# Kernel optimization log

Hardware: AMD Instinct MI355X
Metric: run time of the kernel (lower is better)

The kernel has to match this reference:

```python
import jax, jax.numpy as jnp
import numpy as np


def setup_inputs() -> dict:
    key = jax.random.key(0)
    k1, k2 = jax.random.split(key)
    mat_1 = jax.random.normal(k1, (8192, 128), dtype=jnp.float32)
    mat_2 = jax.random.normal(k2, (8192, 128), dtype=jnp.float32)
    return {"mat_1": mat_1, "mat_2": mat_2}


def reference(mat_1, mat_2):
    # Squared Euclidean distance between every row of mat_1 and every row of mat_2.
    # Same math as sum((mat_1[i] - mat_2[j])**2) but expressed via the
    # ||a||^2 + ||b||^2 - 2 a.b identity so the [n1, n2, d] intermediate is
    # never materialized (single GEMM + rank-1 broadcasts).
    sq1 = jnp.sum(mat_1 * mat_1, axis=1, keepdims=True)        # [n1, 1]
    sq2 = jnp.sum(mat_2 * mat_2, axis=1)                        # [n2]
    cross = jnp.einsum('id,jd->ij', mat_1, mat_2)               # [n1, n2]
    return sq1 + sq2[None, :] - 2.0 * cross
```

## Files before the change

### kernel.cpp

```cpp
#include <hip/hip_runtime.h>


typedef __attribute__((ext_vector_type(8))) short bf16x8;
typedef __attribute__((ext_vector_type(4))) float f32x4;

__device__ __forceinline__ short f2bf(float f) {
    union { float f; unsigned u; } x; x.f = f;
    unsigned r = x.u + 0x7FFFu + ((x.u >> 16) & 1u);
    return (short)(r >> 16);
}

__global__ void norms_kernel(const float* __restrict__ m1,
                             const float* __restrict__ m2,
                             float* __restrict__ n1,
                             float* __restrict__ n2,
                             int rows1, int rows2) {
    int gwave = (int)((blockIdx.x * blockDim.x + threadIdx.x) >> 6);
    int lane  = threadIdx.x & 63;
    const float* src;
    float* dst;
    int row;
    if (gwave < rows1) { src = m1; dst = n1; row = gwave; }
    else {
        row = gwave - rows1;
        if (row >= rows2) return;
        src = m2; dst = n2;
    }
    const float2* p = (const float2*)(src + (size_t)row * 128);
    float2 v = p[lane];
    float s = v.x * v.x + v.y * v.y;
#pragma unroll
    for (int off = 32; off; off >>= 1) s += __shfl_xor(s, off, 64);
    if (lane == 0) dst[row] = s;
}

#define BM 128
#define BN 128
#define BK 64

__global__ __launch_bounds__(256, 3)
void dist_kernel(const float* __restrict__ A, const float* __restrict__ B,
                 const float* __restrict__ n1, const float* __restrict__ n2,
                 float* __restrict__ out, int N2) {
    __shared__ short As[BM][BK];
    __shared__ short Bs[BN][BK];

    const int tid  = threadIdx.x;
    const int wave = tid >> 6;
    const int lane = tid & 63;
    const int q    = lane >> 4;
    const int l15  = lane & 15;

    const int ti = blockIdx.y * BM;
    const int tj = blockIdx.x * BN;

    const int wm = (wave >> 1) * 64;
    const int wn = (wave & 1) * 64;

    f32x4 acc[4][4] = {};

    for (int kc = 0; kc < 128; kc += BK) {
#pragma unroll
        for (int g = 0; g < 4; ++g) {
            int idx = tid + g * 256;
            int row = idx >> 3;
            int kg  = (idx & 7) * 8;
            const float4* pa = (const float4*)(A + (size_t)(ti + row) * 128 + kc + kg);
            float4 v0 = pa[0], v1 = pa[1];
            bf16x8 w;
            w[0] = f2bf(v0.x); w[1] = f2bf(v0.y); w[2] = f2bf(v0.z); w[3] = f2bf(v0.w);
            w[4] = f2bf(v1.x); w[5] = f2bf(v1.y); w[6] = f2bf(v1.z); w[7] = f2bf(v1.w);
            *(bf16x8*)&As[row][kg] = w;
        }
#pragma unroll
        for (int g = 0; g < 4; ++g) {
            int idx = tid + g * 256;
            int row = idx >> 3;
            int kg  = (idx & 7) * 8;
            const float4* pb = (const float4*)(B + (size_t)(tj + row) * 128 + kc + kg);
            float4 v0 = pb[0], v1 = pb[1];
            bf16x8 w;
            w[0] = f2bf(v0.x); w[1] = f2bf(v0.y); w[2] = f2bf(v0.z); w[3] = f2bf(v0.w);
            w[4] = f2bf(v1.x); w[5] = f2bf(v1.y); w[6] = f2bf(v1.z); w[7] = f2bf(v1.w);
            *(bf16x8*)&Bs[row][kg] = w;
        }
        __syncthreads();

#pragma unroll
        for (int kk = 0; kk < BK; kk += 32) {
            bf16x8 af[4], bfr[4];
#pragma unroll
            for (int mi = 0; mi < 4; ++mi)
                af[mi] = *(const bf16x8*)&As[wm + mi * 16 + l15][kk + q * 8];
#pragma unroll
            for (int ni = 0; ni < 4; ++ni)
                bfr[ni] = *(const bf16x8*)&Bs[wn + ni * 16 + l15][kk + q * 8];
#pragma unroll
            for (int mi = 0; mi < 4; ++mi)
#pragma unroll
                for (int ni = 0; ni < 4; ++ni)
                    acc[mi][ni] = __builtin_amdgcn_mfma_f32_16x16x32_bf16(
                        af[mi], bfr[ni], acc[mi][ni], 0, 0, 0);
        }
        __syncthreads();
    }

#pragma unroll
    for (int mi = 0; mi < 4; ++mi) {
        int r0 = ti + wm + mi * 16 + q * 4;
        float a0 = n1[r0 + 0], a1 = n1[r0 + 1], a2 = n1[r0 + 2], a3 = n1[r0 + 3];
#pragma unroll
        for (int ni = 0; ni < 4; ++ni) {
            int c = tj + wn + ni * 16 + l15;
            float nb = n2[c];
            f32x4 v = acc[mi][ni];
            out[(size_t)(r0 + 0) * N2 + c] = a0 + nb - 2.0f * v[0];
            out[(size_t)(r0 + 1) * N2 + c] = a1 + nb - 2.0f * v[1];
            out[(size_t)(r0 + 2) * N2 + c] = a2 + nb - 2.0f * v[2];
            out[(size_t)(r0 + 3) * N2 + c] = a3 + nb - 2.0f * v[3];
        }
    }
}

extern "C" void kernel_launch(void* const* d_in, const int* in_sizes, int n_in,
                              void* d_out, int out_size, void* d_ws, size_t ws_size,
                              hipStream_t stream) {
    const float* m1 = (const float*)d_in[0];
    const float* m2 = (const float*)d_in[1];
    float* out = (float*)d_out;
    const int rows1 = in_sizes[0] / 128;
    const int rows2 = in_sizes[1] / 128;

    float* n1 = (float*)d_ws;
    float* n2 = n1 + rows1;

    int total_waves = rows1 + rows2;
    int nb = (total_waves * 64 + 255) / 256;
    norms_kernel<<<nb, 256, 0, stream>>>(m1, m2, n1, n2, rows1, rows2);

    dim3 grid(rows2 / BN, rows1 / BM);
    dist_kernel<<<grid, 256, 0, stream>>>(m1, m2, n1, n2, out, rows2);
}
```

Baseline: 272.6 us.

## Pre-convert inputs to bf16 in prep kernel and stage tiles via direct global-to-LDS loads

The norms kernel now also writes bf16 copies of both input matrices into the workspace. The distance kernel then loads those copies straight into shared memory with global_load_lds, which drops the per-tile fp32 loads, the conversion arithmetic and the register round trip. Because each input row is re-read by 64 tiles, this halves the bytes fetched per tile and frees VGPRs. In exchange it costs an extra 4MB of bf16 writes in the prep pass and hardcodes the output row stride at 8192.

New measurement: 285.9 us. +4.9%, slower.

```diff
diff --git a/kernel.cpp b/kernel.cpp
--- a/kernel.cpp
+++ b/kernel.cpp
@@ -4,34 +4,38 @@
 typedef __attribute__((ext_vector_type(8))) short bf16x8;
 typedef __attribute__((ext_vector_type(4))) float f32x4;
 
-__device__ __forceinline__ short f2bf(float f) {
+typedef __attribute__((address_space(1))) const void gvoid_t;
+typedef __attribute__((address_space(3))) void lvoid_t;
+
+__device__ __forceinline__ unsigned short f2bf(float f) {
     union { float f; unsigned u; } x; x.f = f;
     unsigned r = x.u + 0x7FFFu + ((x.u >> 16) & 1u);
-    return (short)(r >> 16);
+    return (unsigned short)(r >> 16);
 }
 
-__global__ void norms_kernel(const float* __restrict__ m1,
-                             const float* __restrict__ m2,
-                             float* __restrict__ n1,
-                             float* __restrict__ n2,
-                             int rows1, int rows2) {
+__global__ void prep_kernel(const float* __restrict__ m1,
+                            const float* __restrict__ m2,
+                            unsigned short* __restrict__ A2,
+                            unsigned short* __restrict__ B2,
+                            float* __restrict__ n1,
+                            float* __restrict__ n2,
+                            int rows1, int rows2) {
     int gwave = (int)((blockIdx.x * blockDim.x + threadIdx.x) >> 6);
     int lane  = threadIdx.x & 63;
-    const float* src;
-    float* dst;
-    int row;
-    if (gwave < rows1) { src = m1; dst = n1; row = gwave; }
+    const float* src; unsigned short* dst; float* nd; int row;
+    if (gwave < rows1) { src = m1; dst = A2; nd = n1; row = gwave; }
     else {
         row = gwave - rows1;
         if (row >= rows2) return;
-        src = m2; dst = n2;
+        src = m2; dst = B2; nd = n2;
     }
-    const float2* p = (const float2*)(src + (size_t)row * 128);
-    float2 v = p[lane];
+    float2 v = ((const float2*)(src + (size_t)row * 128))[lane];
     float s = v.x * v.x + v.y * v.y;
+    ushort2 w; w.x = f2bf(v.x); w.y = f2bf(v.y);
+    ((ushort2*)(dst + (size_t)row * 128))[lane] = w;
 #pragma unroll
     for (int off = 32; off; off >>= 1) s += __shfl_xor(s, off, 64);
-    if (lane == 0) dst[row] = s;
+    if (lane == 0) nd[row] = s;
 }
 
 #define BM 128
@@ -39,11 +43,12 @@
 #define BK 64
 
 __global__ __launch_bounds__(256, 3)
-void dist_kernel(const float* __restrict__ A, const float* __restrict__ B,
+void dist_kernel(const unsigned short* __restrict__ A2,
+                 const unsigned short* __restrict__ B2,
                  const float* __restrict__ n1, const float* __restrict__ n2,
-                 float* __restrict__ out, int N2) {
-    __shared__ short As[BM][BK];
-    __shared__ short Bs[BN][BK];
+                 float* __restrict__ out) {
+    __shared__ __align__(16) unsigned short As[BM * BK];
+    __shared__ __align__(16) unsigned short Bs[BN * BK];
 
     const int tid  = threadIdx.x;
     const int wave = tid >> 6;
@@ -57,32 +62,27 @@
     const int wm = (wave >> 1) * 64;
     const int wn = (wave & 1) * 64;
 
+    const int srow   = lane >> 3;
+    const int schunk = lane & 7;
+
     f32x4 acc[4][4] = {};
 
     for (int kc = 0; kc < 128; kc += BK) {
 #pragma unroll
-        for (int g = 0; g < 4; ++g) {
-            int idx = tid + g * 256;
-            int row = idx >> 3;
-            int kg  = (idx & 7) * 8;
-            const float4* pa = (const float4*)(A + (size_t)(ti + row) * 128 + kc + kg);
-            float4 v0 = pa[0], v1 = pa[1];
-            bf16x8 w;
-            w[0] = f2bf(v0.x); w[1] = f2bf(v0.y); w[2] = f2bf(v0.z); w[3] = f2bf(v0.w);
-            w[4] = f2bf(v1.x); w[5] = f2bf(v1.y); w[6] = f2bf(v1.z); w[7] = f2bf(v1.w);
-            *(bf16x8*)&As[row][kg] = w;
+        for (int t = 0; t < 4; ++t) {
+            int i = wave * 4 + t;
+            int row = i * 8 + srow;
+            const unsigned short* g = A2 + (size_t)(ti + row) * 128 + kc + schunk * 8;
+            unsigned short* l = As + i * 512;
+            __builtin_amdgcn_global_load_lds((gvoid_t*)g, (lvoid_t*)l, 16, 0, 0);
         }
 #pragma unroll
-        for (int g = 0; g < 4; ++g) {
-            int idx = tid + g * 256;
-            int row = idx >> 3;
-            int kg  = (idx & 7) * 8;
-            const float4* pb = (const float4*)(B + (size_t)(tj + row) * 128 + kc + kg);
-            float4 v0 = pb[0], v1 = pb[1];
-            bf16x8 w;
-            w[0] = f2bf(v0.x); w[1] = f2bf(v0.y); w[2] = f2bf(v0.z); w[3] = f2bf(v0.w);
-            w[4] = f2bf(v1.x); w[5] = f2bf(v1.y); w[6] = f2bf(v1.z); w[7] = f2bf(v1.w);
-            *(bf16x8*)&Bs[row][kg] = w;
+        for (int t = 0; t < 4; ++t) {
+            int i = wave * 4 + t;
+            int row = i * 8 + srow;
+            const unsigned short* g = B2 + (size_t)(tj + row) * 128 + kc + schunk * 8;
+            unsigned short* l = Bs + i * 512;
+            __builtin_amdgcn_global_load_lds((gvoid_t*)g, (lvoid_t*)l, 16, 0, 0);
         }
         __syncthreads();
 
@@ -91,10 +91,10 @@
             bf16x8 af[4], bfr[4];
 #pragma unroll
             for (int mi = 0; mi < 4; ++mi)
-                af[mi] = *(const bf16x8*)&As[wm + mi * 16 + l15][kk + q * 8];
+                af[mi] = *(const bf16x8*)&As[(wm + mi * 16 + l15) * BK + kk + q * 8];
 #pragma unroll
             for (int ni = 0; ni < 4; ++ni)
-                bfr[ni] = *(const bf16x8*)&Bs[wn + ni * 16 + l15][kk + q * 8];
+                bfr[ni] = *(const bf16x8*)&Bs[(wn + ni * 16 + l15) * BK + kk + q * 8];
 #pragma unroll
             for (int mi = 0; mi < 4; ++mi)
 #pragma unroll
@@ -114,10 +114,10 @@
             int c = tj + wn + ni * 16 + l15;
             float nb = n2[c];
             f32x4 v = acc[mi][ni];
-            out[(size_t)(r0 + 0) * N2 + c] = a0 + nb - 2.0f * v[0];
-            out[(size_t)(r0 + 1) * N2 + c] = a1 + nb - 2.0f * v[1];
-            out[(size_t)(r0 + 2) * N2 + c] = a2 + nb - 2.0f * v[2];
-            out[(size_t)(r0 + 3) * N2 + c] = a3 + nb - 2.0f * v[3];
+            out[(size_t)(r0 + 0) * 8192 + c] = a0 + nb - 2.0f * v[0];
+            out[(size_t)(r0 + 1) * 8192 + c] = a1 + nb - 2.0f * v[1];
+            out[(size_t)(r0 + 2) * 8192 + c] = a2 + nb - 2.0f * v[2];
+            out[(size_t)(r0 + 3) * 8192 + c] = a3 + nb - 2.0f * v[3];
         }
     }
 }
@@ -133,11 +133,13 @@
 
     float* n1 = (float*)d_ws;
     float* n2 = n1 + rows1;
+    unsigned short* A2 = (unsigned short*)(n2 + rows2);
+    unsigned short* B2 = A2 + (size_t)rows1 * 128;
 
     int total_waves = rows1 + rows2;
     int nb = (total_waves * 64 + 255) / 256;
-    norms_kernel<<<nb, 256, 0, stream>>>(m1, m2, n1, n2, rows1, rows2);
+    prep_kernel<<<nb, 256, 0, stream>>>(m1, m2, A2, B2, n1, n2, rows1, rows2);
 
     dim3 grid(rows2 / BN, rows1 / BM);
-    dist_kernel<<<grid, 256, 0, stream>>>(m1, m2, n1, n2, out, rows2);
+    dist_kernel<<<grid, 256, 0, stream>>>(A2, B2, n1, n2, out);
 }
```
